# Optimization experiments

Hardware: AMD Instinct MI355X
Metric: run time of the kernel (lower is better)

The kernel has to match this reference:

```python
import jax, jax.numpy as jnp
from jax import lax
import numpy as np

A = 9            # anchors per location (3 scales x 3 ratios)
STRIDE = 16      # feat_stride
PRE_NMS = 6000   # top-k proposals before NMS (test mode)
POST_NMS = 300   # proposals kept after NMS (test mode)
NMS_T = 0.7      # NMS IoU threshold
MIN_SIZE = 16.0  # min proposal side length


def _anchor_ref(base=16, ratios=(0.5, 1.0, 2.0), scales=(8, 16, 32)):
    """Standard py-faster-rcnn anchor references, shape (9, 4)."""
    ratios = np.array(ratios, np.float64)
    scales = np.array(scales, np.float64)
    ctr = (base - 1) / 2.0
    size = float(base * base)
    ws = np.round(np.sqrt(size / ratios))
    hs = np.round(ws * ratios)
    ra = np.stack([ctr - 0.5 * (ws - 1), ctr - 0.5 * (hs - 1),
                   ctr + 0.5 * (ws - 1), ctr + 0.5 * (hs - 1)], 1)
    out = []
    for a in ra:
        w = a[2] - a[0] + 1.0
        h = a[3] - a[1] + 1.0
        cx = a[0] + 0.5 * (w - 1)
        cy = a[1] + 0.5 * (h - 1)
        ws2 = w * scales
        hs2 = h * scales
        out.append(np.stack([cx - 0.5 * (ws2 - 1), cy - 0.5 * (hs2 - 1),
                             cx + 0.5 * (ws2 - 1), cy + 0.5 * (hs2 - 1)], 1))
    return jnp.asarray(np.concatenate(out, 0), jnp.float32)


def _nms_keep(boxes):
    """Greedy NMS on score-sorted boxes (N,4) -> bool keep mask (N,)."""
    x1, y1, x2, y2 = boxes[:, 0], boxes[:, 1], boxes[:, 2], boxes[:, 3]
    areas = (x2 - x1 + 1.0) * (y2 - y1 + 1.0)
    iw = jnp.clip(jnp.minimum(x2[:, None], x2[None, :]) - jnp.maximum(x1[:, None], x1[None, :]) + 1.0, 0.0)
    ih = jnp.clip(jnp.minimum(y2[:, None], y2[None, :]) - jnp.maximum(y1[:, None], y1[None, :]) + 1.0, 0.0)
    inter = iw * ih
    iou = inter / (areas[:, None] + areas[None, :] - inter)
    n = boxes.shape[0]
    idx = jnp.arange(n)
    def body(i, keep):
        sup = (iou[i] > NMS_T) & (idx > i)
        return jnp.where(keep[i], keep & ~sup, keep)
    return lax.fori_loop(0, n, body, jnp.ones((n,), bool))


def _rpn_forward(feature_map, W_rpn, b_rpn, W_score, b_score, W_bbox, b_bbox, img_size):
    dn = ('NHWC', 'HWIO', 'NHWC')
    rpn = lax.conv_general_dilated(feature_map, W_rpn, (1, 1), 'SAME', dimension_numbers=dn) + b_rpn
    rpn = jax.nn.relu(rpn)
    cls = lax.conv_general_dilated(rpn, W_score, (1, 1), 'SAME', dimension_numbers=dn) + b_score
    bbx = lax.conv_general_dilated(rpn, W_bbox, (1, 1), 'SAME', dimension_numbers=dn) + b_bbox
    n, h, w, _ = feature_map.shape
    cls = cls.reshape(n, h, w, A, 2)
    prob = jax.nn.softmax(cls, axis=-1)
    fg = prob[..., 1].reshape(-1)           # (h*w*A,) foreground prob
    deltas = bbx.reshape(-1, 4)             # (h*w*A, 4)
    # anchors: shifts over (h, w), anchor-ref inner -> matches (h,w,A) flattening
    ref = _anchor_ref()
    sx = jnp.arange(w, dtype=jnp.float32) * STRIDE
    sy = jnp.arange(h, dtype=jnp.float32) * STRIDE
    ys, xs = jnp.meshgrid(sy, sx, indexing='ij')
    shifts = jnp.stack([xs, ys, xs, ys], -1).reshape(-1, 1, 4)
    anchors = (shifts + ref[None]).reshape(-1, 4)
    # decode deltas -> boxes
    aw = anchors[:, 2] - anchors[:, 0] + 1.0
    ah = anchors[:, 3] - anchors[:, 1] + 1.0
    acx = anchors[:, 0] + 0.5 * aw
    acy = anchors[:, 1] + 0.5 * ah
    pcx = deltas[:, 0] * aw + acx
    pcy = deltas[:, 1] * ah + acy
    pw = jnp.exp(deltas[:, 2]) * aw
    ph = jnp.exp(deltas[:, 3]) * ah
    imh = img_size[0].astype(jnp.float32)
    imw = img_size[1].astype(jnp.float32)
    boxes = jnp.stack([
        jnp.clip(pcx - 0.5 * pw, 0.0, imw - 1.0),
        jnp.clip(pcy - 0.5 * ph, 0.0, imh - 1.0),
        jnp.clip(pcx + 0.5 * pw, 0.0, imw - 1.0),
        jnp.clip(pcy + 0.5 * ph, 0.0, imh - 1.0)], -1)
    # min-size filter
    bw = boxes[:, 2] - boxes[:, 0] + 1.0
    bh = boxes[:, 3] - boxes[:, 1] + 1.0
    fg = jnp.where((bw >= MIN_SIZE) & (bh >= MIN_SIZE), fg, -1e9)
    # pre-NMS top-k (sorted descending)
    top_s, top_i = lax.top_k(fg, PRE_NMS)
    top_b = boxes[top_i]
    keep = _nms_keep(lax.stop_gradient(top_b))
    sel_s = jnp.where(keep, top_s, -1e9)
    _, sel_i = lax.top_k(sel_s, POST_NMS)
    rois = top_b[sel_i]
    ok = keep[sel_i] & (sel_s[sel_i] > -1e8)
    return jnp.where(ok[:, None], rois, 0.0)  # (POST_NMS, 4), zero-padded


def setup_inputs() -> dict:
    key = jax.random.key(0)
    ks = jax.random.split(key, 7)
    C_in, C_mid = 1024, 512
    std = 0.01
    return {
        'feature_map': jax.random.normal(ks[0], (1, 100, 150, C_in), jnp.float32),
        'W_rpn': jax.random.normal(ks[1], (3, 3, C_in, C_mid), jnp.float32) * std,
        'b_rpn': jnp.zeros((C_mid,), jnp.float32),
        'W_score': jax.random.normal(ks[2], (1, 1, C_mid, A * 2), jnp.float32) * std,
        'b_score': jnp.zeros((A * 2,), jnp.float32),
        'W_bbox': jax.random.normal(ks[3], (1, 1, C_mid, A * 4), jnp.float32) * std,
        'b_bbox': jnp.zeros((A * 4,), jnp.float32),
        'img_size': jnp.array([1600, 2400], jnp.int32),
    }


def reference(feature_map, W_rpn, b_rpn, W_score, b_score, W_bbox, b_bbox, img_size):
    return _rpn_forward(feature_map, W_rpn, b_rpn, W_score, b_score, W_bbox, b_bbox, img_size)
```

## Files before the change

kernel.cpp:

```cpp
#include <hip/hip_runtime.h>
#include <hip/hip_bf16.h>

typedef unsigned int u32;
typedef unsigned long long u64;

#define H_FM 100
#define W_FM 150
#define CIN 1024
#define CMID 512
#define NPIX 15000
#define NANCH 135000
#define PRE_NMS_N 6000
#define POST_NMS_N 300
#define WPR 94

#define PW 152
#define PH 104
#define PPIX (PW * PH)
#define CHSZ ((u64)PPIX * 64)
#define ASPLIT (32 * CHSZ)
#define BSPLIT ((u64)9216 * 512 * 2)

typedef __attribute__((ext_vector_type(8))) short short8;
typedef __attribute__((ext_vector_type(8))) __bf16 bf16x8;
typedef __attribute__((ext_vector_type(4))) float f32x4;

__device__ __forceinline__ u32 fkey(float f) {
  u32 u = __float_as_uint(f);
  return (u & 0x80000000u) ? ~u : (u | 0x80000000u);
}

__device__ __forceinline__ u64 shfl64(u64 v, int src) {
  u32 lo = (u32)__shfl((int)(u32)v, src, 64);
  u32 hi = (u32)__shfl((int)(u32)(v >> 32), src, 64);
  return ((u64)hi << 32) | (u64)lo;
}

struct FragArg {
  short8 v;
  __device__ operator short8() const { return v; }
  __device__ operator bf16x8() const { return __builtin_bit_cast(bf16x8, v); }
};
__device__ __forceinline__ f32x4 mfma16(short8 a, short8 b, f32x4 c) {
  return __builtin_amdgcn_mfma_f32_16x16x32_bf16(FragArg{a}, FragArg{b}, c, 0, 0, 0);
}

#define GLL(gp, lp) __builtin_amdgcn_global_load_lds(                        \
    (const __attribute__((address_space(1))) unsigned int*)(gp),             \
    (__attribute__((address_space(3))) unsigned int*)(lp), 16, 0, 0)

__device__ __forceinline__ void split3(float f, unsigned short& a,
                                       unsigned short& b, unsigned short& c) {
  __hip_bfloat16 h0 = __float2bfloat16(f);
  float f0 = __bfloat162float(h0);
  float r1 = f - f0;
  __hip_bfloat16 h1 = __float2bfloat16(r1);
  float r2 = r1 - __bfloat162float(h1);
  __hip_bfloat16 h2 = __float2bfloat16(r2);
  a = *(unsigned short*)&h0;
  b = *(unsigned short*)&h1;
  c = *(unsigned short*)&h2;
}

__global__ __launch_bounds__(256) void k_splitA(
    const float* __restrict__ src, unsigned short* __restrict__ Ap)
{
  const int id = blockIdx.x * 256 + threadIdx.x;
  if (id < 3 * 32 * 808) {
    int sc = id / 808, h = id - sc * 808;
    int s = sc >> 5, c = sc & 31;
    int pp;
    if (h < 152) pp = h;
    else if (h < 608) pp = 101 * 152 + (h - 152);
    else { int k = h - 608; pp = ((k >> 1) + 1) * 152 + ((k & 1) ? 151 : 0); }
    float4* dst = (float4*)((char*)Ap + (u64)s * ASPLIT + (u64)c * CHSZ + (u64)pp * 64);
    float4 zz = make_float4(0.f, 0.f, 0.f, 0.f);
    dst[0] = zz; dst[1] = zz; dst[2] = zz; dst[3] = zz;
  }
  if (id >= 32 * NPIX) return;
  const int c = id / NPIX;
  const int p = id - c * NPIX;
  const float* s8 = src + (size_t)p * 1024 + c * 32;
  float f[32];
  #pragma unroll
  for (int q = 0; q < 8; ++q) *(float4*)&f[q * 4] = *(const float4*)(s8 + q * 4);
  unsigned short o0[32], o1[32], o2[32];
  #pragma unroll
  for (int e = 0; e < 32; ++e) split3(f[e], o0[e], o1[e], o2[e]);
  const int yy = p / 150;
  const int pp = (yy + 1) * 152 + (p - yy * 150) + 1;
  const u64 off = (u64)c * CHSZ + (u64)pp * 64;
  #pragma unroll
  for (int q = 0; q < 8; ++q) {
    *(ushort4*)((char*)Ap + off + q * 8)              = *(ushort4*)&o0[q * 4];
    *(ushort4*)((char*)Ap + ASPLIT + off + q * 8)     = *(ushort4*)&o1[q * 4];
    *(ushort4*)((char*)Ap + 2 * ASPLIT + off + q * 8) = *(ushort4*)&o2[q * 4];
  }
}

__global__ __launch_bounds__(256) void k_splitB(
    const float* __restrict__ Wsrc, unsigned short* __restrict__ Bp)
{
  __shared__ float tile[64][65];
  const int k0 = blockIdx.x * 64;
  const int n0 = blockIdx.y * 64;
  const int tid = threadIdx.x;
  const int lr = tid >> 4;
  const int lc = (tid & 15) * 4;
  #pragma unroll
  for (int rr = 0; rr < 64; rr += 16) {
    float4 v = *(const float4*)&Wsrc[(size_t)(k0 + lr + rr) * CMID + n0 + lc];
    tile[lr + rr][lc + 0] = v.x; tile[lr + rr][lc + 1] = v.y;
    tile[lr + rr][lc + 2] = v.z; tile[lr + rr][lc + 3] = v.w;
  }
  __syncthreads();
  const int n = n0 + (tid >> 2);
  const int kk = k0 + (tid & 3) * 16;
  unsigned short b0[16], b1[16], b2[16];
  #pragma unroll
  for (int e = 0; e < 16; ++e)
    split3(tile[(tid & 3) * 16 + e][tid >> 2], b0[e], b1[e], b2[e]);
  const int nblk = n >> 7, row = n & 127;
  const int seg = kk >> 10, chunk = (kk >> 5) & 31, ch = kk & 31;
  u64 base = ((u64)((nblk * 9 + seg) * 32 + chunk)) * 8192 + row * 64 + ch * 2;
  #pragma unroll
  for (int q = 0; q < 4; ++q) {
    *(ushort4*)((char*)Bp + base + q * 8) = *(ushort4*)&b0[q * 4];
    *(ushort4*)((char*)Bp + BSPLIT + base + q * 8) = *(ushort4*)&b1[q * 4];
    *(ushort4*)((char*)Bp + 2 * BSPLIT + base + q * 8) = *(ushort4*)&b2[q * 4];
  }
}

__global__ __launch_bounds__(256, 2) void k_conv8(
    const unsigned short* __restrict__ Ap, const unsigned short* __restrict__ Bp,
    const float* __restrict__ br, float* __restrict__ rpn)
{
  __shared__ char lds[49152];
  const int gb = blockIdx.x;
  const int xcd = gb & 7;
  const int nblk = (gb >> 3) & 3;
  const int bmi = (gb >> 5) * 8 + xcd;
  if (bmi >= 118) return;
  const int bn = nblk * 128;
  const int bm = bmi * 128;
  const int tid = threadIdx.x;
  const int L = tid & 63;
  const int w = tid >> 6;
  const int wm = (w >> 1) * 64, wn = (w & 1) * 64;

  const int r = L >> 2;
  const u32 dqb = (u32)(((L & 3) ^ ((r >> 1) & 3)) * 16);

  int ay[2], ax[2];
  {
    int m0 = bm + w * 16 + r;       ay[0] = m0 / 150; ax[0] = m0 - ay[0] * 150;
    int m1 = bm + (w + 4) * 16 + r; ay[1] = m1 / 150; ax[1] = m1 - ay[1] * 150;
  }
  const u32 brow0 = (u32)((w * 16 + r) * 64) + dqb;
  const u32 brow1 = (u32)(((w + 4) * 16 + r) * 64) + dqb;
  const u64 bbase = (u64)nblk * 9 * 32 * 8192;

  const int fr = L & 15, fq = L >> 4;
  const u32 fsw = (u32)((fq ^ ((fr >> 1) & 3)) * 16);
  const u32 aF = (u32)((wm >> 4) * 1024 + fr * 64) + fsw;
  const u32 bF = 24576u + (u32)((wn >> 4) * 1024 + fr * 64) + fsw;

  u32 apix[2];
  auto segSetup = [&](int seg) {
    int dy = seg / 3 - 1, dx = seg - (seg / 3) * 3 - 1;
    apix[0] = (u32)(((ay[0] + dy + 1) * 152 + ax[0] + dx + 1) * 64) + dqb;
    apix[1] = (u32)(((ay[1] + dy + 1) * 152 + ax[1] + dx + 1) * 64) + dqb;
  };

  auto stage = [&](int seg, int chunk) {
    const u64 ach = (u64)chunk * CHSZ;
    #pragma unroll
    for (int s = 0; s < 3; ++s) {
      const char* as = (const char*)Ap + (u64)s * ASPLIT + ach;
      GLL(as + apix[0], lds + s * 8192 + w * 1024);
      GLL(as + apix[1], lds + s * 8192 + (w + 4) * 1024);
    }
    const u64 bch = bbase + (u64)(seg * 32 + chunk) * 8192;
    #pragma unroll
    for (int s = 0; s < 3; ++s) {
      const char* bs = (const char*)Bp + (u64)s * BSPLIT + bch;
      GLL(bs + brow0, lds + 24576 + s * 8192 + w * 1024);
      GLL(bs + brow1, lds + 24576 + s * 8192 + (w + 4) * 1024);
    }
  };

  short8 Af[3][4], Bf[3][4];
  auto readFrags = [&]() {
    #pragma unroll
    for (int s = 0; s < 3; ++s)
      #pragma unroll
      for (int i = 0; i < 4; ++i) {
        Af[s][i] = *(const short8*)(lds + aF + s * 8192 + i * 1024);
        Bf[s][i] = *(const short8*)(lds + bF + s * 8192 + i * 1024);
      }
  };

  f32x4 acc[4][4];
  #pragma unroll
  for (int i = 0; i < 4; ++i)
    #pragma unroll
    for (int j = 0; j < 4; ++j) acc[i][j] = (f32x4){0.f, 0.f, 0.f, 0.f};

  segSetup(0);
  stage(0, 0);
  __syncthreads();
  readFrags();

  for (int it = 0; it < 288; ++it) {
    const int nit = it + 1;
    const bool more = nit < 288;
    if (more && (nit & 31) == 0) segSetup(nit >> 5);
    __syncthreads();
    if (more) stage(nit >> 5, nit & 31);
    #pragma unroll
    for (int i = 0; i < 4; ++i)
      #pragma unroll
      for (int j = 0; j < 4; ++j) {
        f32x4 c = acc[i][j];
        c = mfma16(Af[0][i], Bf[0][j], c);
        c = mfma16(Af[0][i], Bf[1][j], c);
        c = mfma16(Af[1][i], Bf[0][j], c);
        c = mfma16(Af[1][i], Bf[1][j], c);
        c = mfma16(Af[0][i], Bf[2][j], c);
        c = mfma16(Af[2][i], Bf[0][j], c);
        acc[i][j] = c;
      }
    __syncthreads();
    if (more) readFrags();
  }

  #pragma unroll
  for (int i = 0; i < 4; ++i) {
    const int mb = bm + wm + i * 16 + ((L >> 4) << 2);
    #pragma unroll
    for (int ri = 0; ri < 4; ++ri) {
      const int m = mb + ri;
      if (m < NPIX) {
        float* op = rpn + (size_t)m * CMID;
        #pragma unroll
        for (int j = 0; j < 4; ++j) {
          const int n = bn + wn + j * 16 + (L & 15);
          op[n] = fmaxf(acc[i][j][ri] + br[n], 0.f);
        }
      }
    }
  }
}

__global__ __launch_bounds__(256) void k_packW(
    const float* __restrict__ Ws, const float* __restrict__ bs,
    const float* __restrict__ Wb, const float* __restrict__ bb,
    float* __restrict__ Wp, float* __restrict__ bp,
    u32* __restrict__ hist, u32* __restrict__ ctl)
{
  int tt = blockIdx.x * 256 + threadIdx.x;
  int k = tt >> 6, o = tt & 63;
  float v = (o < 18) ? Ws[k * 18 + o] : ((o < 54) ? Wb[k * 36 + (o - 18)] : 0.f);
  Wp[tt] = v;
  if (tt < 64) bp[tt] = (tt < 18) ? bs[tt] : ((tt < 54) ? bb[tt - 18] : 0.f);
  if (tt < 256) hist[tt] = 0;
  if (tt < 16) ctl[tt] = 0;
  if (tt == 1) ctl[1] = PRE_NMS_N;
}

__global__ __launch_bounds__(256) void k_headdec(
    const float* __restrict__ rpn, const float* __restrict__ Wp,
    const float* __restrict__ bp, const int* __restrict__ img,
    float* __restrict__ fg, float4* __restrict__ boxes)
{
  __shared__ float As[32][33];
  __shared__ float Bs[32][64];
  __shared__ float vs[32 * 64];
  const int tid = threadIdx.x;
  const int bm = blockIdx.x * 32;
  const int r  = tid >> 3;
  const int kg = tid & 7;
  const int c8 = (tid & 7) * 8;
  const int n4 = (tid & 15) * 4;
  const int kr = tid >> 4;
  const float4 z4 = make_float4(0.f, 0.f, 0.f, 0.f);

  float acc[8];
  #pragma unroll
  for (int j = 0; j < 8; ++j) acc[j] = 0.f;

  for (int kc = 0; kc < 512; kc += 32) {
    __syncthreads();
    {
      int m = bm + r;
      float4 v = (m < NPIX) ? *(const float4*)&rpn[(size_t)m * CMID + kc + kg * 4] : z4;
      As[kg * 4 + 0][r] = v.x; As[kg * 4 + 1][r] = v.y;
      As[kg * 4 + 2][r] = v.z; As[kg * 4 + 3][r] = v.w;
    }
    *(float4*)&Bs[kr][n4]      = *(const float4*)&Wp[(kc + kr) * 64 + n4];
    *(float4*)&Bs[kr + 16][n4] = *(const float4*)&Wp[(kc + kr + 16) * 64 + n4];
    __syncthreads();
    #pragma unroll
    for (int kk = 0; kk < 32; ++kk) {
      float a = As[kk][r];
      float4 b0 = *(const float4*)&Bs[kk][c8];
      float4 b1 = *(const float4*)&Bs[kk][c8 + 4];
      acc[0] = fmaf(a, b0.x, acc[0]); acc[1] = fmaf(a, b0.y, acc[1]);
      acc[2] = fmaf(a, b0.z, acc[2]); acc[3] = fmaf(a, b0.w, acc[3]);
      acc[4] = fmaf(a, b1.x, acc[4]); acc[5] = fmaf(a, b1.y, acc[5]);
      acc[6] = fmaf(a, b1.z, acc[6]); acc[7] = fmaf(a, b1.w, acc[7]);
    }
  }
  __syncthreads();
  #pragma unroll
  for (int j = 0; j < 8; ++j) vs[r * 64 + c8 + j] = acc[j] + bp[c8 + j];
  __syncthreads();

  const float AW[9] = {184.f, 368.f, 736.f, 128.f, 256.f, 512.f,  88.f, 176.f, 352.f};
  const float AH[9] = { 96.f, 192.f, 384.f, 128.f, 256.f, 512.f, 176.f, 352.f, 704.f};
  const float imh1 = (float)img[0] - 1.f;
  const float imw1 = (float)img[1] - 1.f;
  for (int id = tid; id < 32 * 9; id += 256) {
    int pl = id / 9, a = id - pl * 9;
    int p = bm + pl;
    if (p >= NPIX) break;
    const float* row = vs + pl * 64;
    const int y = p / W_FM, x = p - y * W_FM;

    float c0 = row[2 * a], c1 = row[2 * a + 1];
    float score = 1.f / (1.f + expf(c0 - c1));

    float dxv = row[18 + 4 * a + 0];
    float dyv = row[18 + 4 * a + 1];
    float dwv = row[18 + 4 * a + 2];
    float dhv = row[18 + 4 * a + 3];

    float aw = AW[a], ah = AH[a];
    float acx = (float)(x * 16 + 8);
    float acy = (float)(y * 16 + 8);
    float pcx = dxv * aw + acx;
    float pcy = dyv * ah + acy;
    float pw = expf(dwv) * aw;
    float ph = expf(dhv) * ah;

    float b0 = fminf(fmaxf(pcx - 0.5f * pw, 0.f), imw1);
    float b1 = fminf(fmaxf(pcy - 0.5f * ph, 0.f), imh1);
    float b2 = fminf(fmaxf(pcx + 0.5f * pw, 0.f), imw1);
    float b3 = fminf(fmaxf(pcy + 0.5f * ph, 0.f), imh1);

    float bw = b2 - b0 + 1.f, bh = b3 - b1 + 1.f;
    if (!(bw >= 16.f && bh >= 16.f)) score = -1e9f;

    int gi = p * 9 + a;
    fg[gi] = score;
    boxes[gi] = make_float4(b0, b1, b2, b3);
  }
}

__global__ __launch_bounds__(256) void k_hist(
    const float* __restrict__ fg, u32* __restrict__ hist,
    const u32* __restrict__ ctl, int pass)
{
  __shared__ u32 h[256];
  h[threadIdx.x] = 0;
  __syncthreads();
  const int shift = 24 - 8 * pass;
  const u32 prefix = ctl[0];
  for (int i = blockIdx.x * 256 + threadIdx.x; i < NANCH; i += 128 * 256) {
    u32 key = fkey(fg[i]);
    bool match = (pass == 0) || ((key >> (shift + 8)) == prefix);
    if (match) atomicAdd(&h[(key >> shift) & 255], 1u);
  }
  __syncthreads();
  u32 c = h[threadIdx.x];
  if (c) atomicAdd(&hist[threadIdx.x], c);
}

__global__ void k_scan(u32* __restrict__ hist, u32* __restrict__ ctl) {
  if (threadIdx.x == 0) {
    u32 kneed = ctl[1];
    u32 cum = 0;
    int d = 0;
    for (int dd = 255; dd >= 0; --dd) {
      u32 c = hist[dd];
      if (cum + c >= kneed) { d = dd; break; }
      cum += c;
    }
    ctl[0] = (ctl[0] << 8) | (u32)d;
    ctl[1] = kneed - cum;
  }
  __syncthreads();
  hist[threadIdx.x] = 0;
}

__global__ __launch_bounds__(256) void k_compact(
    const float* __restrict__ fg, u32* __restrict__ ctl,
    u64* __restrict__ listA, u32* __restrict__ listB)
{
  int i = blockIdx.x * 256 + threadIdx.x;
  if (i >= NANCH) return;
  u32 T = ctl[0];
  u32 key = fkey(fg[i]);
  if (key > T) {
    u32 slot = atomicAdd(&ctl[2], 1u);
    listA[slot] = ((u64)key << 32) | (u64)(0xFFFFFFFFu - (u32)i);
  } else if (key == T) {
    u32 slot = atomicAdd(&ctl[3], 1u);
    if (slot < 8192) listB[slot] = (u32)i;
  }
}

__global__ __launch_bounds__(256) void k_tiefix(
    u32* __restrict__ ctl, const u32* __restrict__ listB, u64* __restrict__ listA)
{
  __shared__ u32 s[8192];
  const int tid = threadIdx.x;
  const u32 kneed = ctl[1];
  const u32 base = ctl[2];
  const u32 cntB = min(ctl[3], 8192u);
  const u32 T = ctl[0];
  if (kneed == 0) return;
  if (cntB == kneed) {
    for (u32 t = tid; t < kneed; t += 256)
      listA[base + t] = ((u64)T << 32) | (u64)(0xFFFFFFFFu - listB[t]);
    return;
  }
  u32 n2 = 1;
  while (n2 < cntB) n2 <<= 1;
  for (u32 i = tid; i < n2; i += 256) s[i] = (i < cntB) ? listB[i] : 0xFFFFFFFFu;
  __syncthreads();
  for (u32 k = 2; k <= n2; k <<= 1) {
    for (u32 j = k >> 1; j > 0; j >>= 1) {
      for (u32 i = tid; i < n2; i += 256) {
        u32 ixj = i ^ j;
        if (ixj > i) {
          u32 a = s[i], b = s[ixj];
          bool up = ((i & k) == 0);
          if ((a > b) == up) { s[i] = b; s[ixj] = a; }
        }
      }
      __syncthreads();
    }
  }
  for (u32 t = tid; t < kneed; t += 256)
    listA[base + t] = ((u64)T << 32) | (u64)(0xFFFFFFFFu - s[t]);
}

__global__ __launch_bounds__(1024) void k_sort(
    const u64* __restrict__ listA, u64* __restrict__ sorted)
{
  __shared__ u64 s[8192];
  const int tid = threadIdx.x;
  for (int i = tid; i < 8192; i += 1024) s[i] = (i < PRE_NMS_N) ? listA[i] : 0ull;
  __syncthreads();
  for (int k = 2; k <= 8192; k <<= 1) {
    for (int j = k >> 1; j > 0; j >>= 1) {
      for (int i = tid; i < 8192; i += 1024) {
        int ixj = i ^ j;
        if (ixj > i) {
          u64 a = s[i], b = s[ixj];
          bool up = ((i & k) == 0);
          if ((a < b) == up) { s[i] = b; s[ixj] = a; }
        }
      }
      __syncthreads();
    }
  }
  for (int i = tid; i < 8192; i += 1024) sorted[i] = s[i];
}

__global__ __launch_bounds__(256) void k_gather(
    const u64* __restrict__ sorted, const float4* __restrict__ boxes,
    float4* __restrict__ tb, u32* __restrict__ ctl)
{
  int t = blockIdx.x * 256 + threadIdx.x;
  const u32 kcut = fkey(-1e8f);
  bool inb = t < PRE_NMS_N;
  u64 p = inb ? sorted[t] : 0ull;
  bool valid = inb && ((u32)(p >> 32) > kcut);
  u64 ball = __ballot(valid);
  if ((threadIdx.x & 63) == 0 && ball) atomicAdd(&ctl[8], (u32)__popcll(ball));
  if (!inb) return;
  u32 idx = 0xFFFFFFFFu - (u32)(p & 0xFFFFFFFFull);
  tb[t] = boxes[idx];
}

__global__ __launch_bounds__(64) void k_mask(
    const float4* __restrict__ tb, u64* __restrict__ mask)
{
  __shared__ float4 cb[64];
  const int bj = blockIdx.x, bi = blockIdx.y, t = threadIdx.x;
  const int j0 = bj * 64;
  const int jn = min(64, PRE_NMS_N - j0);
  if (t < jn) cb[t] = tb[j0 + t];
  __syncthreads();
  const int i = bi * 64 + t;
  if (i >= PRE_NMS_N) return;
  const float4 b = tb[i];
  const float ai = (b.z - b.x + 1.f) * (b.w - b.y + 1.f);
  u64 bits = 0;
  for (int tt = 0; tt < jn; ++tt) {
    int j = j0 + tt;
    if (j <= i) continue;
    float4 c = cb[tt];
    float iw = fminf(b.z, c.z) - fmaxf(b.x, c.x) + 1.f;
    float ih = fminf(b.w, c.w) - fmaxf(b.y, c.y) + 1.f;
    float inter = fmaxf(iw, 0.f) * fmaxf(ih, 0.f);
    float aj = (c.z - c.x + 1.f) * (c.w - c.y + 1.f);
    float iou = inter / (ai + aj - inter);
    if (iou > 0.7f) bits |= (1ull << tt);
  }
  mask[(size_t)i * WPR + bj] = bits;
}

__global__ __launch_bounds__(64) void k_nms(
    const u64* __restrict__ mask, const float* __restrict__ tb,
    const u32* __restrict__ ctl, float* __restrict__ out)
{
  const int lane = threadIdx.x;
  const int nvalid = min((int)ctl[8], PRE_NMS_N);
  u64 r0 = 0, r1 = 0;
  int kept = 0;
  for (int w = 0; w < WPR && kept < POST_NMS_N; ++w) {
    const int base = w << 6;
    if (base >= nvalid) break;
    u64 rw = (w < 64) ? shfl64(r0, w) : shfl64(r1, w - 64);
    u64 live = ~rw;
    if (base + 64 > nvalid) live &= ((1ull << (nvalid - base)) - 1ull);
    while (live) {
      int b = (int)(__ffsll((long long)live) - 1);
      int i = base + b;
      if (lane < 4) out[kept * 4 + lane] = tb[i * 4 + lane];
      ++kept;
      if (kept >= POST_NMS_N) break;
      const u64* row = mask + (size_t)i * WPR;
      u64 m0 = row[lane];
      u64 m1 = (lane < WPR - 64) ? row[64 + lane] : 0ull;
      r0 |= m0; r1 |= m1;
      u64 rwi = (w < 64) ? shfl64(m0, w) : shfl64(m1, w - 64);
      live &= ~rwi;
      live = (b == 63) ? 0ull : (live & (~0ull << (b + 1)));
    }
  }
  for (int j = kept * 4 + lane; j < POST_NMS_N * 4; j += 64) out[j] = 0.f;
}

extern "C" void kernel_launch(void* const* d_in, const int* in_sizes, int n_in,
                              void* d_out, int out_size, void* d_ws, size_t ws_size,
                              hipStream_t stream) {
  const float* fm  = (const float*)d_in[0];
  const float* Wr  = (const float*)d_in[1];
  const float* br  = (const float*)d_in[2];
  const float* Wsc = (const float*)d_in[3];
  const float* bsc = (const float*)d_in[4];
  const float* Wbb = (const float*)d_in[5];
  const float* bbb = (const float*)d_in[6];
  const int*   img = (const int*)d_in[7];
  float* out = (float*)d_out;

  char* w = (char*)d_ws;
  size_t off = 0;
  auto alloc = [&](size_t bytes) {
    size_t p = off;
    off = (off + bytes + 255) & ~(size_t)255;
    return p;
  };
  float* rpn    = (float*)(w + alloc((size_t)NPIX * CMID * 4));
  float* fg     = (float*)(w + alloc((size_t)NANCH * 4));
  float4* boxes = (float4*)(w + alloc((size_t)NANCH * 16));
  u32* hist     = (u32*)(w + alloc(1024));
  u32* ctl      = (u32*)(w + alloc(64));
  u64* listA    = (u64*)(w + alloc((size_t)PRE_NMS_N * 8));
  u32* listB    = (u32*)(w + alloc(8192 * 4));
  u64* sorted   = (u64*)(w + alloc(8192 * 8));
  float4* topbox= (float4*)(w + alloc((size_t)PRE_NMS_N * 16));
  u64* mask     = (u64*)(w + alloc((size_t)PRE_NMS_N * WPR * 8));
  float* Wp     = (float*)(w + alloc(512 * 64 * 4));
  float* bp     = (float*)(w + alloc(64 * 4));
  unsigned short* Ap = (unsigned short*)(w + alloc((size_t)(3 * ASPLIT)));
  unsigned short* Bp = (unsigned short*)(w + alloc((size_t)(3 * BSPLIT)));

  k_splitA<<<dim3((32 * NPIX + 255) / 256), dim3(256), 0, stream>>>(fm, Ap);
  k_splitB<<<dim3(144, 8), dim3(256), 0, stream>>>(Wr, Bp);
  k_packW<<<dim3(128), dim3(256), 0, stream>>>(Wsc, bsc, Wbb, bbb, Wp, bp, hist, ctl);
  k_conv8<<<dim3(480), dim3(256), 0, stream>>>(Ap, Bp, br, rpn);
  k_headdec<<<dim3(472), dim3(256), 0, stream>>>(rpn, Wp, bp, img, fg, boxes);
  for (int pass = 0; pass < 4; ++pass) {
    k_hist<<<128, 256, 0, stream>>>(fg, hist, ctl, pass);
    k_scan<<<1, 256, 0, stream>>>(hist, ctl);
  }
  k_compact<<<(NANCH + 255) / 256, 256, 0, stream>>>(fg, ctl, listA, listB);
  k_tiefix<<<1, 256, 0, stream>>>(ctl, listB, listA);
  k_sort<<<1, 1024, 0, stream>>>(listA, sorted);
  k_gather<<<(PRE_NMS_N + 255) / 256, 256, 0, stream>>>(sorted, boxes, topbox, ctl);
  k_mask<<<dim3(WPR, WPR), 64, 0, stream>>>(topbox, mask);
  k_nms<<<1, 64, 0, stream>>>(mask, (const float*)topbox, ctl, out);
}
```

Before: 1.145 ms.

## Fold histogram scan into last-block of k_hist, fuse gather into sort, prefetch NMS rows

```diff
diff --git a/kernel.cpp b/kernel.cpp
--- a/kernel.cpp
+++ b/kernel.cpp
@@ -359,9 +359,10 @@
 
 __global__ __launch_bounds__(256) void k_hist(
     const float* __restrict__ fg, u32* __restrict__ hist,
-    const u32* __restrict__ ctl, int pass)
+    u32* __restrict__ ctl, int pass)
 {
   __shared__ u32 h[256];
+  __shared__ int amLast;
   h[threadIdx.x] = 0;
   __syncthreads();
   const int shift = 24 - 8 * pass;
@@ -374,22 +375,26 @@
   __syncthreads();
   u32 c = h[threadIdx.x];
   if (c) atomicAdd(&hist[threadIdx.x], c);
-}
-
-__global__ void k_scan(u32* __restrict__ hist, u32* __restrict__ ctl) {
+  __threadfence();
+  if (threadIdx.x == 0)
+    amLast = (atomicAdd(&ctl[12 + pass], 1u) == 127u);
+  __syncthreads();
+  if (!amLast) return;
+  __threadfence();
+  h[threadIdx.x] = atomicAdd(&hist[threadIdx.x], 0u);
+  __syncthreads();
   if (threadIdx.x == 0) {
     u32 kneed = ctl[1];
     u32 cum = 0;
     int d = 0;
     for (int dd = 255; dd >= 0; --dd) {
-      u32 c = hist[dd];
-      if (cum + c >= kneed) { d = dd; break; }
-      cum += c;
+      u32 cc = h[dd];
+      if (cum + cc >= kneed) { d = dd; break; }
+      cum += cc;
     }
     ctl[0] = (ctl[0] << 8) | (u32)d;
     ctl[1] = kneed - cum;
   }
-  __syncthreads();
   hist[threadIdx.x] = 0;
 }
 
@@ -447,7 +452,8 @@
 }
 
 __global__ __launch_bounds__(1024) void k_sort(
-    const u64* __restrict__ listA, u64* __restrict__ sorted)
+    const u64* __restrict__ listA, const float4* __restrict__ boxes,
+    float4* __restrict__ tb, u32* __restrict__ ctl)
 {
   __shared__ u64 s[8192];
   const int tid = threadIdx.x;
@@ -466,23 +472,17 @@
       __syncthreads();
     }
   }
-  for (int i = tid; i < 8192; i += 1024) sorted[i] = s[i];
-}
-
-__global__ __launch_bounds__(256) void k_gather(
-    const u64* __restrict__ sorted, const float4* __restrict__ boxes,
-    float4* __restrict__ tb, u32* __restrict__ ctl)
-{
-  int t = blockIdx.x * 256 + threadIdx.x;
   const u32 kcut = fkey(-1e8f);
-  bool inb = t < PRE_NMS_N;
-  u64 p = inb ? sorted[t] : 0ull;
-  bool valid = inb && ((u32)(p >> 32) > kcut);
-  u64 ball = __ballot(valid);
-  if ((threadIdx.x & 63) == 0 && ball) atomicAdd(&ctl[8], (u32)__popcll(ball));
-  if (!inb) return;
-  u32 idx = 0xFFFFFFFFu - (u32)(p & 0xFFFFFFFFull);
-  tb[t] = boxes[idx];
+  u32 nv = 0;
+  for (int i = tid; i < PRE_NMS_N; i += 1024) {
+    u64 p = s[i];
+    if ((u32)(p >> 32) > kcut) ++nv;
+    u32 idx = 0xFFFFFFFFu - (u32)(p & 0xFFFFFFFFull);
+    tb[i] = boxes[idx];
+  }
+  #pragma unroll
+  for (int o = 32; o > 0; o >>= 1) nv += (u32)__shfl_down((int)nv, o, 64);
+  if ((tid & 63) == 0 && nv) atomicAdd(&ctl[8], nv);
 }
 
 __global__ __launch_bounds__(64) void k_mask(
@@ -521,6 +521,8 @@
   const int nvalid = min((int)ctl[8], PRE_NMS_N);
   u64 r0 = 0, r1 = 0;
   int kept = 0;
+  int pidx = -1;
+  u64 p0 = 0, p1 = 0;
   for (int w = 0; w < WPR && kept < POST_NMS_N; ++w) {
     const int base = w << 6;
     if (base >= nvalid) break;
@@ -530,16 +532,26 @@
     while (live) {
       int b = (int)(__ffsll((long long)live) - 1);
       int i = base + b;
+      u64 m0, m1;
+      if (pidx == i) { m0 = p0; m1 = p1; }
+      else {
+        const u64* row = mask + (size_t)i * WPR;
+        m0 = row[lane];
+        m1 = (lane < WPR - 64) ? row[64 + lane] : 0ull;
+      }
+      u64 liveAfter = (b == 63) ? 0ull : (live & (~0ull << (b + 1)));
+      if (liveAfter) {
+        pidx = base + (int)(__ffsll((long long)liveAfter) - 1);
+        const u64* prow = mask + (size_t)pidx * WPR;
+        p0 = prow[lane];
+        p1 = (lane < WPR - 64) ? prow[64 + lane] : 0ull;
+      } else pidx = -1;
       if (lane < 4) out[kept * 4 + lane] = tb[i * 4 + lane];
       ++kept;
       if (kept >= POST_NMS_N) break;
-      const u64* row = mask + (size_t)i * WPR;
-      u64 m0 = row[lane];
-      u64 m1 = (lane < WPR - 64) ? row[64 + lane] : 0ull;
       r0 |= m0; r1 |= m1;
       u64 rwi = (w < 64) ? shfl64(m0, w) : shfl64(m1, w - 64);
-      live &= ~rwi;
-      live = (b == 63) ? 0ull : (live & (~0ull << (b + 1)));
+      live = liveAfter & ~rwi;
     }
   }
   for (int j = kept * 4 + lane; j < POST_NMS_N * 4; j += 64) out[j] = 0.f;
@@ -572,7 +584,6 @@
   u32* ctl      = (u32*)(w + alloc(64));
   u64* listA    = (u64*)(w + alloc((size_t)PRE_NMS_N * 8));
   u32* listB    = (u32*)(w + alloc(8192 * 4));
-  u64* sorted   = (u64*)(w + alloc(8192 * 8));
   float4* topbox= (float4*)(w + alloc((size_t)PRE_NMS_N * 16));
   u64* mask     = (u64*)(w + alloc((size_t)PRE_NMS_N * WPR * 8));
   float* Wp     = (float*)(w + alloc(512 * 64 * 4));
@@ -585,14 +596,11 @@
   k_packW<<<dim3(128), dim3(256), 0, stream>>>(Wsc, bsc, Wbb, bbb, Wp, bp, hist, ctl);
   k_conv8<<<dim3(480), dim3(256), 0, stream>>>(Ap, Bp, br, rpn);
   k_headdec<<<dim3(472), dim3(256), 0, stream>>>(rpn, Wp, bp, img, fg, boxes);
-  for (int pass = 0; pass < 4; ++pass) {
+  for (int pass = 0; pass < 4; ++pass)
     k_hist<<<128, 256, 0, stream>>>(fg, hist, ctl, pass);
-    k_scan<<<1, 256, 0, stream>>>(hist, ctl);
-  }
   k_compact<<<(NANCH + 255) / 256, 256, 0, stream>>>(fg, ctl, listA, listB);
   k_tiefix<<<1, 256, 0, stream>>>(ctl, listB, listA);
-  k_sort<<<1, 1024, 0, stream>>>(listA, sorted);
-  k_gather<<<(PRE_NMS_N + 255) / 256, 256, 0, stream>>>(sorted, boxes, topbox, ctl);
+  k_sort<<<1, 1024, 0, stream>>>(listA, boxes, topbox, ctl);
   k_mask<<<dim3(WPR, WPR), 64, 0, stream>>>(topbox, mask);
   k_nms<<<1, 64, 0, stream>>>(mask, (const float*)topbox, ctl, out);
 }
```

Result: slower. 1.196 ms (+4.5%).
